# Performance work log

Hardware: AMD Instinct MI355X
Metric: run time of the kernel (lower is better)

Reference implementation:

```python
import jax, jax.numpy as jnp
import numpy as np

N_NODES = 50000
N_EDGES = 800000
IN_CH = 128
HID = 256
OUT_CH = 10
N_GRAPHS = 64


def setup_inputs() -> dict:
    key = jax.random.key(0)
    ks = jax.random.split(key, 16)
    s = 0.02
    inp = {
        "x": jax.random.normal(ks[0], (N_NODES, IN_CH), dtype=jnp.float32),
        "edge_index": jax.random.randint(ks[1], (2, N_EDGES), 0, N_NODES, dtype=jnp.int64),
        "batch": jnp.sort(jax.random.randint(ks[2], (N_NODES,), 0, N_GRAPHS, dtype=jnp.int64)),
        # SAGEConv params: out = lin_l(mean_agg) + lin_r(x_root); lin_l has bias, lin_r does not (PyG default)
        "W1l": jax.random.normal(ks[3], (HID, IN_CH), dtype=jnp.float32) * s,
        "b1": jnp.zeros((HID,), jnp.float32),
        "W1r": jax.random.normal(ks[4], (HID, IN_CH), dtype=jnp.float32) * s,
        "W2l": jax.random.normal(ks[5], (HID, HID), dtype=jnp.float32) * s,
        "b2": jnp.zeros((HID,), jnp.float32),
        "W2r": jax.random.normal(ks[6], (HID, HID), dtype=jnp.float32) * s,
        "W3l": jax.random.normal(ks[7], (HID, HID), dtype=jnp.float32) * s,
        "b3": jnp.zeros((HID,), jnp.float32),
        "W3r": jax.random.normal(ks[8], (HID, HID), dtype=jnp.float32) * s,
        "lin1_W": jax.random.normal(ks[9], (HID // 2, HID), dtype=jnp.float32) * s,
        "lin1_b": jnp.zeros((HID // 2,), jnp.float32),
        "lin2_W": jax.random.normal(ks[10], (OUT_CH, HID // 2), dtype=jnp.float32) * s,
        "lin2_b": jnp.zeros((OUT_CH,), jnp.float32),
    }
    return inp


def _sage_conv(x, src, dst, Wl, bl, Wr):
    # mean-aggregate neighbor features at destination nodes
    msg_sum = jax.ops.segment_sum(x[src], dst, num_segments=N_NODES)  # [N, d]
    deg = jax.ops.segment_sum(jnp.ones((src.shape[0],), x.dtype), dst, num_segments=N_NODES)
    agg = msg_sum / jnp.maximum(deg, 1.0)[:, None]
    return agg @ Wl.T + bl + x @ Wr.T


def reference(x, edge_index, batch, W1l, b1, W1r, W2l, b2, W2r, W3l, b3, W3r,
              lin1_W, lin1_b, lin2_W, lin2_b):
    src, dst = edge_index[0], edge_index[1]
    h = jax.nn.relu(_sage_conv(x, src, dst, W1l, b1, W1r))
    h = jax.nn.relu(_sage_conv(h, src, dst, W2l, b2, W2r))
    h = jax.nn.relu(_sage_conv(h, src, dst, W3l, b3, W3r))
    # global_mean_pool over batch vector
    pooled_sum = jax.ops.segment_sum(h, batch, num_segments=N_GRAPHS)  # [G, HID]
    counts = jax.ops.segment_sum(jnp.ones((h.shape[0],), h.dtype), batch, num_segments=N_GRAPHS)
    g = pooled_sum / jnp.maximum(counts, 1.0)[:, None]
    g = jax.nn.relu(g @ lin1_W.T + lin1_b)
    # dropout is identity in eval mode
    return g @ lin2_W.T + lin2_b
```

## Files before the change

kernel.cpp:

```cpp
#include <hip/hip_runtime.h>
#include <hip/hip_bf16.h>


#define HID 256
typedef unsigned short ushort_t;
typedef __bf16 bf16x8 __attribute__((ext_vector_type(8)));
typedef float  f32x4  __attribute__((ext_vector_type(4)));
typedef float  f32x2  __attribute__((ext_vector_type(2)));

__device__ __forceinline__ unsigned short f2bf(float f) {
    unsigned int u = __float_as_uint(f);
    unsigned int r = (u + 0x7fffu + ((u >> 16) & 1u)) >> 16;
    return (unsigned short)r;
}
__device__ __forceinline__ float bflo(unsigned int u) { return __uint_as_float(u << 16); }
__device__ __forceinline__ float bfhi(unsigned int u) { return __uint_as_float(u & 0xffff0000u); }
__device__ __forceinline__ unsigned int packbf(float a, float b) {
    return (unsigned int)f2bf(a) | ((unsigned int)f2bf(b) << 16);
}
__device__ __forceinline__ void gld16(const void* g, void* l) {
    __builtin_amdgcn_global_load_lds(
        (const __attribute__((address_space(1))) unsigned int*)g,
        (__attribute__((address_space(3))) unsigned int*)l, 16, 0, 0);
}
__device__ __forceinline__ void fma8(float* a, float w, const uint4 v) {
    a[0] = fmaf(w, bflo(v.x), a[0]); a[1] = fmaf(w, bfhi(v.x), a[1]);
    a[2] = fmaf(w, bflo(v.y), a[2]); a[3] = fmaf(w, bfhi(v.y), a[3]);
    a[4] = fmaf(w, bflo(v.z), a[4]); a[5] = fmaf(w, bfhi(v.z), a[5]);
    a[6] = fmaf(w, bflo(v.w), a[6]); a[7] = fmaf(w, bfhi(v.w), a[7]);
}
__device__ __forceinline__ void fma8_f8(float* a, float w, const uint2 v) {
    const f32x2 c01 = __builtin_amdgcn_cvt_pk_f32_fp8(v.x, false);
    const f32x2 c23 = __builtin_amdgcn_cvt_pk_f32_fp8(v.x, true);
    const f32x2 c45 = __builtin_amdgcn_cvt_pk_f32_fp8(v.y, false);
    const f32x2 c67 = __builtin_amdgcn_cvt_pk_f32_fp8(v.y, true);
    a[0] = fmaf(w, c01.x, a[0]); a[1] = fmaf(w, c01.y, a[1]);
    a[2] = fmaf(w, c23.x, a[2]); a[3] = fmaf(w, c23.y, a[3]);
    a[4] = fmaf(w, c45.x, a[4]); a[5] = fmaf(w, c45.y, a[5]);
    a[6] = fmaf(w, c67.x, a[6]); a[7] = fmaf(w, c67.y, a[7]);
}
__device__ __forceinline__ int4 load4idx(const int* __restrict__ csr, int pbase, int e1m1) {
    int4 r;
    r.x = csr[min(pbase + 0, e1m1)];
    r.y = csr[min(pbase + 1, e1m1)];
    r.z = csr[min(pbase + 2, e1m1)];
    r.w = csr[min(pbase + 3, e1m1)];
    return r;
}

#define NBUCK 256
#define NPB_BUCK 196
#define BCAP 4096

__global__ __launch_bounds__(256)
void cvt_kernel(const float* __restrict__ x, ushort_t* __restrict__ xb,
                unsigned char* __restrict__ x8, int nx4,
                const float* __restrict__ W1l, const float* __restrict__ W1r,
                const float* __restrict__ W2l, const float* __restrict__ W2r,
                const float* __restrict__ W3l, const float* __restrict__ W3r,
                ushort_t* __restrict__ wdst, int s1, int s2,
                int* __restrict__ bcursor, float* __restrict__ pooled) {
    const int t = blockIdx.x * 256 + threadIdx.x;
    if (t < NBUCK) bcursor[t] = 0;
    if (t < 64 * 256 / 4) *(float4*)(pooled + t * 4) = make_float4(0.f, 0.f, 0.f, 0.f);
    if (t < nx4) {
        const int i = t * 4;
        const float4 v = *(const float4*)(x + i);
        *(uint2*)(xb + i) = make_uint2(packbf(v.x, v.y), packbf(v.z, v.w));
        int p = __builtin_amdgcn_cvt_pk_fp8_f32(v.x, v.y, 0, false);
        p = __builtin_amdgcn_cvt_pk_fp8_f32(v.z, v.w, p, true);
        *(unsigned int*)(x8 + i) = (unsigned int)p;
        return;
    }
    int off = t - nx4;
    const int total = 2 * s1 + 4 * s2;
    if (off >= total) return;
    const int i = off;
    const float* src;
    if (off < s1) src = W1l;
    else if ((off -= s1) < s1) src = W1r;
    else if ((off -= s1) < s2) src = W2l;
    else if ((off -= s2) < s2) src = W2r;
    else if ((off -= s2) < s2) src = W3l;
    else { off -= s2; src = W3r; }
    wdst[i] = f2bf(src[off]);
}

__global__ __launch_bounds__(256)
void binA_kernel(const int* __restrict__ src, const int* __restrict__ dst,
                 int* __restrict__ bcursor, unsigned int* __restrict__ staging, int E) {
    __shared__ int hist[NBUCK];
    __shared__ int wbase[NBUCK];
    const int tid = threadIdx.x;
    hist[tid] = 0;
    __syncthreads();
    const int i0 = blockIdx.x * 2048;
    int d8[8], s8[8], b8[8];
    #pragma unroll
    for (int j = 0; j < 8; ++j) {
        const int i = i0 + j * 256 + tid;
        if (i < E) {
            d8[j] = dst[i];
            s8[j] = src[i];
            b8[j] = d8[j] / NPB_BUCK;
            atomicAdd(&hist[b8[j]], 1);
        } else b8[j] = -1;
    }
    __syncthreads();
    {
        const int b = tid;
        const int cnt = hist[b];
        int wb = 0;
        if (cnt > 0) wb = atomicAdd(&bcursor[b], cnt);
        wbase[b] = b * BCAP + wb;
        hist[b] = 0;
    }
    __syncthreads();
    #pragma unroll
    for (int j = 0; j < 8; ++j) {
        if (b8[j] >= 0) {
            const int pos = wbase[b8[j]] + atomicAdd(&hist[b8[j]], 1);
            if (pos < (b8[j] + 1) * BCAP)
                staging[pos] = ((unsigned int)(d8[j] - b8[j] * NPB_BUCK) << 16) | (unsigned int)s8[j];
        }
    }
}

__global__ __launch_bounds__(256)
void binB_kernel(const unsigned int* __restrict__ staging, const int* __restrict__ bcursor,
                 int* __restrict__ csr, int* __restrict__ offsets, int nn, int E) {
    __shared__ unsigned int sedge[BCAP];
    __shared__ int cnt[NBUCK];
    __shared__ int bsum[4];
    __shared__ int wt[4];
    const int b = blockIdx.x, tid = threadIdx.x;
    const int lane = tid & 63, wid = tid >> 6;

    int part = (tid < b) ? bcursor[tid] : 0;
    #pragma unroll
    for (int d = 1; d < 64; d <<= 1) part += __shfl_xor(part, d, 64);
    if (lane == 0) bsum[wid] = part;
    const int mycnt = min(bcursor[b], BCAP);
    __syncthreads();
    const int base = bsum[0] + bsum[1] + bsum[2] + bsum[3];

    for (int i = tid; i < mycnt; i += 256) sedge[i] = staging[b * BCAP + i];
    cnt[tid] = 0;
    __syncthreads();
    for (int i = tid; i < mycnt; i += 256) atomicAdd(&cnt[sedge[i] >> 16], 1);
    __syncthreads();

    const int v = cnt[tid];
    int incl = v;
    #pragma unroll
    for (int d = 1; d < 64; d <<= 1) {
        int t = __shfl_up(incl, d, 64);
        if (lane >= d) incl += t;
    }
    if (lane == 63) wt[wid] = incl;
    __syncthreads();
    int wb = 0;
    #pragma unroll
    for (int w = 0; w < 4; ++w) { int t = wt[w]; if (w < wid) wb += t; }
    const int excl = wb + incl - v;

    const int node = b * NPB_BUCK + tid;
    if (tid < NPB_BUCK && node < nn) offsets[node] = base + excl;
    if (b == NBUCK - 1 && tid == 0) offsets[nn] = E;
    __syncthreads();
    cnt[tid] = excl;
    __syncthreads();

    for (int i = tid; i < mycnt; i += 256) {
        const unsigned int e = sedge[i];
        const int p = atomicAdd(&cnt[e >> 16], 1);
        csr[base + p] = (int)(e & 0xFFFFu);
    }
}

template <int C>
__global__ __launch_bounds__(256)
void agg8_kernel(const unsigned char* __restrict__ h8, const int* __restrict__ offsets,
                 const int* __restrict__ csr, ushort_t* __restrict__ out, int nn) {
    constexpr int CL = C / 8;
    constexpr int EW = 64 / CL;
    constexpr int RPE = 4 * EW;
    const int node = (blockIdx.x * 256 + threadIdx.x) >> 6;
    if (node >= nn) return;
    const int lane = threadIdx.x & 63;
    const int cl = lane & (CL - 1);
    const int eo = lane / CL;
    const int e0 = offsets[node], e1 = offsets[node + 1];
    const int deg = e1 - e0;
    const int rounds = (deg + RPE - 1) / RPE;
    const int e1m1 = max(e1 - 1, 0);
    float a[8] = {0.f, 0.f, 0.f, 0.f, 0.f, 0.f, 0.f, 0.f};
    int pb = e0 + eo * 4;
    if (rounds > 0) {
        int4 idx = load4idx(csr, pb, e1m1);
        for (int r2 = 0; r2 < rounds; ++r2) {
            const int4 cur = idx;
            const int pcur = pb;
            pb += RPE;
            if (r2 + 1 < rounds) idx = load4idx(csr, pb, e1m1);
            const uint2 v0 = *(const uint2*)(h8 + (size_t)cur.x * C + cl * 8);
            const uint2 v1 = *(const uint2*)(h8 + (size_t)cur.y * C + cl * 8);
            const uint2 v2 = *(const uint2*)(h8 + (size_t)cur.z * C + cl * 8);
            const uint2 v3 = *(const uint2*)(h8 + (size_t)cur.w * C + cl * 8);
            fma8_f8(a, (pcur + 0 < e1) ? 1.f : 0.f, v0);
            fma8_f8(a, (pcur + 1 < e1) ? 1.f : 0.f, v1);
            fma8_f8(a, (pcur + 2 < e1) ? 1.f : 0.f, v2);
            fma8_f8(a, (pcur + 3 < e1) ? 1.f : 0.f, v3);
        }
    }
    #pragma unroll
    for (int d = CL; d < 64; d <<= 1)
        #pragma unroll
        for (int r = 0; r < 8; ++r) a[r] += __shfl_xor(a[r], d, 64);
    if (eo == 0) {
        const float inv = 1.0f / fmaxf((float)deg, 1.0f);
        uint4 o;
        o.x = packbf(a[0] * inv, a[1] * inv);
        o.y = packbf(a[2] * inv, a[3] * inv);
        o.z = packbf(a[4] * inv, a[5] * inv);
        o.w = packbf(a[6] * inv, a[7] * inv);
        *(uint4*)(out + (size_t)node * C + cl * 8) = o;
    }
}

template <int K, bool W8>
__global__ __launch_bounds__(256, 2)
void gemm2_mfma(const ushort_t* __restrict__ A1, const ushort_t* __restrict__ A2,
                const ushort_t* __restrict__ W1, const ushort_t* __restrict__ W2,
                const float* __restrict__ bias, ushort_t* __restrict__ Cout,
                unsigned char* __restrict__ H8, int M) {
    __shared__ ushort_t As[2 * 128 * 64];
    __shared__ ushort_t Bs[2 * 128 * 64];
    const int tid = threadIdx.x;
    const int row0 = blockIdx.x * 128, col0 = blockIdx.y * 128;
    const int wave = tid >> 6, lane = tid & 63;
    const int wm = (wave & 1) * 64, wn = (wave >> 1) * 64;
    const int l15 = lane & 15, quad = lane >> 4;
    constexpr int NCH = K / 128;

    f32x4 acc[4][4] = {};

    #pragma unroll
    for (int phase = 0; phase < 2; ++phase) {
        const ushort_t* __restrict__ A = phase ? A2 : A1;
        const ushort_t* __restrict__ W = phase ? W2 : W1;
        for (int kc = 0; kc < NCH; ++kc) {
            const int kt = kc * 128;
            __syncthreads();
            #pragma unroll
            for (int p = 0; p < 8; ++p) {
                const int slot = p * 256 + tid;
                const int g = slot >> 10;
                const int r = (slot >> 3) & 127;
                const int c = slot & 7;
                const int cg = c ^ (r & 7);
                int ar = row0 + r; if (ar >= M) ar = M - 1;
                gld16(A + (size_t)ar * K + kt + g * 64 + cg * 8, &As[slot * 8]);
            }
            #pragma unroll
            for (int p = 0; p < 8; ++p) {
                const int slot = p * 256 + tid;
                const int g = slot >> 10;
                const int r = (slot >> 3) & 127;
                const int c = slot & 7;
                const int cg = c ^ (r & 7);
                gld16(W + (size_t)(col0 + r) * K + kt + g * 64 + cg * 8, &Bs[slot * 8]);
            }
            __syncthreads();
            #pragma unroll
            for (int g = 0; g < 2; ++g) {
                #pragma unroll
                for (int ks = 0; ks < 2; ++ks) {
                    const int kq = ks * 4 + quad;
                    bf16x8 af[4], bfv[4];
                    #pragma unroll
                    for (int i = 0; i < 4; ++i) {
                        const int r = wm + i * 16 + l15;
                        const int cl = kq ^ (r & 7);
                        af[i] = *(const bf16x8*)&As[g * 8192 + r * 64 + cl * 8];
                    }
                    #pragma unroll
                    for (int j = 0; j < 4; ++j) {
                        const int r = wn + j * 16 + l15;
                        const int cl = kq ^ (r & 7);
                        bfv[j] = *(const bf16x8*)&Bs[g * 8192 + r * 64 + cl * 8];
                    }
                    #pragma unroll
                    for (int i = 0; i < 4; ++i)
                        #pragma unroll
                        for (int j = 0; j < 4; ++j)
                            acc[i][j] = __builtin_amdgcn_mfma_f32_16x16x32_bf16(
                                af[i], bfv[j], acc[i][j], 0, 0, 0);
                }
            }
        }
    }

    #pragma unroll
    for (int i = 0; i < 4; ++i) {
        const int mbase = row0 + wm + i * 16 + quad * 4;
        #pragma unroll
        for (int j = 0; j < 4; ++j) {
            const int n = col0 + wn + j * 16 + l15;
            const float b = bias[n];
            #pragma unroll
            for (int reg = 0; reg < 4; ++reg) {
                const int mr = mbase + reg;
                const float v = fmaxf(acc[i][j][reg] + b, 0.f);
                const float vp = __shfl_xor(v, 1, 64);
                if (!(l15 & 1) && mr < M)
                    *(unsigned int*)(Cout + (size_t)mr * 256 + n) = packbf(v, vp);
                if (W8) {
                    const int p2 = __builtin_amdgcn_cvt_pk_fp8_f32(v, vp, 0, false);
                    const int q2 = __shfl_xor(p2, 2, 64);
                    if ((l15 & 3) == 0 && mr < M)
                        *(unsigned int*)(H8 + (size_t)mr * 256 + n) =
                            ((unsigned int)p2 & 0xFFFFu) | ((unsigned int)q2 << 16);
                }
            }
        }
    }
}

__global__ __launch_bounds__(256)
void pool_partial_kernel(const ushort_t* __restrict__ h, const int* __restrict__ batch,
                         float* __restrict__ pooled, int nn) {
    const int n0 = blockIdx.x * 64;
    if (n0 >= nn) return;
    const int n1 = min(n0 + 64, nn);
    const int tid = threadIdx.x;
    const int cl = tid & 31, rg = tid >> 5;
    const int g0 = batch[n0];
    const int g1 = batch[n1 - 1];
    float a0[8] = {0.f, 0.f, 0.f, 0.f, 0.f, 0.f, 0.f, 0.f};
    float a1[8] = {0.f, 0.f, 0.f, 0.f, 0.f, 0.f, 0.f, 0.f};
    for (int n = n0 + rg; n < n1; n += 8) {
        const uint4 v = *(const uint4*)(h + (size_t)n * 256 + cl * 8);
        const float w1 = (batch[n] != g0) ? 1.f : 0.f;
        fma8(a0, 1.f - w1, v);
        fma8(a1, w1, v);
    }
    __shared__ float red[8][512];
    #pragma unroll
    for (int r = 0; r < 8; ++r) {
        red[rg][cl * 8 + r] = a0[r];
        red[rg][256 + cl * 8 + r] = a1[r];
    }
    __syncthreads();
    float s0 = 0.f, s1 = 0.f;
    #pragma unroll
    for (int r = 0; r < 8; ++r) { s0 += red[r][tid]; s1 += red[r][256 + tid]; }
    atomicAdd(&pooled[g0 * 256 + tid], s0);
    if (g1 != g0) atomicAdd(&pooled[g1 * 256 + tid], s1);
}

__global__ __launch_bounds__(256)
void mlp_kernel(const float* __restrict__ pooled, const int* __restrict__ batch, int nn,
                const float* __restrict__ lin1W, const float* __restrict__ lin1b,
                const float* __restrict__ lin2W, const float* __restrict__ lin2b,
                float* __restrict__ out) {
    const int g = blockIdx.x;
    const int tid = threadIdx.x;
    int lo = 0, hi = nn;
    while (lo < hi) { int mid = (lo + hi) >> 1; if (batch[mid] < g) lo = mid + 1; else hi = mid; }
    const int s = lo;
    hi = nn;
    while (lo < hi) { int mid = (lo + hi) >> 1; if (batch[mid] < g + 1) lo = mid + 1; else hi = mid; }
    const int e = lo;
    __shared__ float meanv[256];
    __shared__ float g1v[128];
    meanv[tid] = pooled[g * 256 + tid] / fmaxf((float)(e - s), 1.0f);
    __syncthreads();
    if (tid < 128) {
        float acc = lin1b[tid];
        #pragma unroll 4
        for (int k = 0; k < 256; k += 4) {
            const float4 w = *(const float4*)(lin1W + tid * 256 + k);
            acc += meanv[k] * w.x + meanv[k + 1] * w.y + meanv[k + 2] * w.z + meanv[k + 3] * w.w;
        }
        g1v[tid] = fmaxf(acc, 0.f);
    }
    __syncthreads();
    if (tid < 10) {
        float o = lin2b[tid];
        #pragma unroll 4
        for (int k = 0; k < 128; k += 4) {
            const float4 w = *(const float4*)(lin2W + tid * 128 + k);
            o += g1v[k] * w.x + g1v[k + 1] * w.y + g1v[k + 2] * w.z + g1v[k + 3] * w.w;
        }
        out[g * 10 + tid] = o;
    }
}

extern "C" void kernel_launch(void* const* d_in, const int* in_sizes, int n_in,
                              void* d_out, int out_size, void* d_ws, size_t ws_size,
                              hipStream_t stream) {
    const float* x     = (const float*)d_in[0];
    const int*   eidx  = (const int*)d_in[1];
    const int*   batch = (const int*)d_in[2];
    const float* W1l = (const float*)d_in[3];
    const float* b1  = (const float*)d_in[4];
    const float* W1r = (const float*)d_in[5];
    const float* W2l = (const float*)d_in[6];
    const float* b2  = (const float*)d_in[7];
    const float* W2r = (const float*)d_in[8];
    const float* W3l = (const float*)d_in[9];
    const float* b3  = (const float*)d_in[10];
    const float* W3r = (const float*)d_in[11];
    const float* lin1W = (const float*)d_in[12];
    const float* lin1b = (const float*)d_in[13];
    const float* lin2W = (const float*)d_in[14];
    const float* lin2b = (const float*)d_in[15];
    float* out = (float*)d_out;

    const int E  = in_sizes[1] / 2;
    const int NN = in_sizes[2];
    const int IN = 128;
    const int* src = eidx;
    const int* dst = eidx + E;

    char* ws = (char*)d_ws;
    size_t off = 0;
    auto alloc = [&](size_t bytes) { void* p = ws + off; off += (bytes + 255) / 256 * 256; return p; };
    ushort_t* xb  = (ushort_t*)alloc((size_t)NN * IN * 2);
    unsigned char* x8 = (unsigned char*)alloc((size_t)NN * IN);
    ushort_t* agg = (ushort_t*)alloc((size_t)NN * HID * 2);
    ushort_t* hA  = (ushort_t*)alloc((size_t)NN * HID * 2);
    ushort_t* hB  = (ushort_t*)alloc((size_t)NN * HID * 2);
    unsigned char* h8 = (unsigned char*)alloc((size_t)NN * HID);
    const int s1 = HID * IN, s2 = HID * HID;
    ushort_t* wb  = (ushort_t*)alloc((size_t)(2 * s1 + 4 * s2) * 2);
    int* offsets   = (int*)alloc((size_t)(NN + 1) * 4);
    int* csr       = (int*)alloc((size_t)E * 4);
    unsigned int* staging = (unsigned int*)alloc((size_t)NBUCK * BCAP * 4);
    int* bcursor   = (int*)alloc(NBUCK * 4);
    float* pooled  = (float*)alloc(64 * 256 * 4);
    (void)ws_size; (void)n_in; (void)out_size;

    const ushort_t* W1lb = wb;
    const ushort_t* W1rb = wb + s1;
    const ushort_t* W2lb = wb + 2 * s1;
    const ushort_t* W2rb = wb + 2 * s1 + s2;
    const ushort_t* W3lb = wb + 2 * s1 + 2 * s2;
    const ushort_t* W3rb = wb + 2 * s1 + 3 * s2;

    const int TB = 256;
    const int mgrid = (NN + 127) / 128;

    const int nx4 = NN * IN / 4;
    const int wtotal = 2 * s1 + 4 * s2;
    cvt_kernel<<<(nx4 + wtotal + TB - 1) / TB, TB, 0, stream>>>(
        x, xb, x8, nx4, W1l, W1r, W2l, W2r, W3l, W3r, wb, s1, s2, bcursor, pooled);

    binA_kernel<<<(E + 2047) / 2048, TB, 0, stream>>>(src, dst, bcursor, staging, E);
    binB_kernel<<<NBUCK, TB, 0, stream>>>(staging, bcursor, csr, offsets, NN, E);

    agg8_kernel<128><<<(NN + 3) / 4, TB, 0, stream>>>(x8, offsets, csr, agg, NN);
    gemm2_mfma<128, true><<<dim3(mgrid, 2), TB, 0, stream>>>(agg, xb, W1lb, W1rb, b1, hA, h8, NN);
    agg8_kernel<256><<<(NN + 3) / 4, TB, 0, stream>>>(h8, offsets, csr, agg, NN);
    gemm2_mfma<256, true><<<dim3(mgrid, 2), TB, 0, stream>>>(agg, hA, W2lb, W2rb, b2, hB, h8, NN);
    agg8_kernel<256><<<(NN + 3) / 4, TB, 0, stream>>>(h8, offsets, csr, agg, NN);
    gemm2_mfma<256, false><<<dim3(mgrid, 2), TB, 0, stream>>>(agg, hB, W3lb, W3rb, b3, hA, nullptr, NN);

    pool_partial_kernel<<<(NN + 63) / 64, TB, 0, stream>>>(hA, batch, pooled, NN);
    mlp_kernel<<<64, TB, 0, stream>>>(pooled, batch, NN, lin1W, lin1b, lin2W, lin2b, out);
}
```

Before: 324.8 us.

## Store all activations and aggregates in fp8, decode to bf16 inside GEMM

Switches every intermediate tensor (aggregates, root features, layer outputs) from bf16 to fp8 storage. The GEMM now loads fp8 A tiles into a smaller LDS buffer and decodes them to bf16 before the MFMA, which cuts A-operand traffic and LDS use and allows raising occupancy to 3 blocks per CU. This drops the dual bf16/fp8 writes in the epilogue and the bf16 copy of x. It adds decode ALU work in the inner loop and lowers precision of the root-path and final activations, which risks accuracy.

```diff
diff --git a/kernel.cpp b/kernel.cpp
--- a/kernel.cpp
+++ b/kernel.cpp
@@ -22,12 +22,6 @@
     __builtin_amdgcn_global_load_lds(
         (const __attribute__((address_space(1))) unsigned int*)g,
         (__attribute__((address_space(3))) unsigned int*)l, 16, 0, 0);
-}
-__device__ __forceinline__ void fma8(float* a, float w, const uint4 v) {
-    a[0] = fmaf(w, bflo(v.x), a[0]); a[1] = fmaf(w, bfhi(v.x), a[1]);
-    a[2] = fmaf(w, bflo(v.y), a[2]); a[3] = fmaf(w, bfhi(v.y), a[3]);
-    a[4] = fmaf(w, bflo(v.z), a[4]); a[5] = fmaf(w, bfhi(v.z), a[5]);
-    a[6] = fmaf(w, bflo(v.w), a[6]); a[7] = fmaf(w, bfhi(v.w), a[7]);
 }
 __device__ __forceinline__ void fma8_f8(float* a, float w, const uint2 v) {
     const f32x2 c01 = __builtin_amdgcn_cvt_pk_f32_fp8(v.x, false);
@@ -39,6 +33,18 @@
     a[4] = fmaf(w, c45.x, a[4]); a[5] = fmaf(w, c45.y, a[5]);
     a[6] = fmaf(w, c67.x, a[6]); a[7] = fmaf(w, c67.y, a[7]);
 }
+__device__ __forceinline__ bf16x8 dec8(const uint2 v) {
+    const f32x2 c01 = __builtin_amdgcn_cvt_pk_f32_fp8(v.x, false);
+    const f32x2 c23 = __builtin_amdgcn_cvt_pk_f32_fp8(v.x, true);
+    const f32x2 c45 = __builtin_amdgcn_cvt_pk_f32_fp8(v.y, false);
+    const f32x2 c67 = __builtin_amdgcn_cvt_pk_f32_fp8(v.y, true);
+    uint4 u;
+    u.x = packbf(c01.x, c01.y);
+    u.y = packbf(c23.x, c23.y);
+    u.z = packbf(c45.x, c45.y);
+    u.w = packbf(c67.x, c67.y);
+    return *(bf16x8*)&u;
+}
 __device__ __forceinline__ int4 load4idx(const int* __restrict__ csr, int pbase, int e1m1) {
     int4 r;
     r.x = csr[min(pbase + 0, e1m1)];
@@ -53,8 +59,7 @@
 #define BCAP 4096
 
 __global__ __launch_bounds__(256)
-void cvt_kernel(const float* __restrict__ x, ushort_t* __restrict__ xb,
-                unsigned char* __restrict__ x8, int nx4,
+void cvt_kernel(const float* __restrict__ x, unsigned char* __restrict__ x8, int nx4,
                 const float* __restrict__ W1l, const float* __restrict__ W1r,
                 const float* __restrict__ W2l, const float* __restrict__ W2r,
                 const float* __restrict__ W3l, const float* __restrict__ W3r,
@@ -66,7 +71,6 @@
     if (t < nx4) {
         const int i = t * 4;
         const float4 v = *(const float4*)(x + i);
-        *(uint2*)(xb + i) = make_uint2(packbf(v.x, v.y), packbf(v.z, v.w));
         int p = __builtin_amdgcn_cvt_pk_fp8_f32(v.x, v.y, 0, false);
         p = __builtin_amdgcn_cvt_pk_fp8_f32(v.z, v.w, p, true);
         *(unsigned int*)(x8 + i) = (unsigned int)p;
@@ -181,7 +185,7 @@
 template <int C>
 __global__ __launch_bounds__(256)
 void agg8_kernel(const unsigned char* __restrict__ h8, const int* __restrict__ offsets,
-                 const int* __restrict__ csr, ushort_t* __restrict__ out, int nn) {
+                 const int* __restrict__ csr, unsigned char* __restrict__ out, int nn) {
     constexpr int CL = C / 8;
     constexpr int EW = 64 / CL;
     constexpr int RPE = 4 * EW;
@@ -219,22 +223,20 @@
         for (int r = 0; r < 8; ++r) a[r] += __shfl_xor(a[r], d, 64);
     if (eo == 0) {
         const float inv = 1.0f / fmaxf((float)deg, 1.0f);
-        uint4 o;
-        o.x = packbf(a[0] * inv, a[1] * inv);
-        o.y = packbf(a[2] * inv, a[3] * inv);
-        o.z = packbf(a[4] * inv, a[5] * inv);
-        o.w = packbf(a[6] * inv, a[7] * inv);
-        *(uint4*)(out + (size_t)node * C + cl * 8) = o;
-    }
-}
-
-template <int K, bool W8>
-__global__ __launch_bounds__(256, 2)
-void gemm2_mfma(const ushort_t* __restrict__ A1, const ushort_t* __restrict__ A2,
+        int p = __builtin_amdgcn_cvt_pk_fp8_f32(a[0] * inv, a[1] * inv, 0, false);
+        p = __builtin_amdgcn_cvt_pk_fp8_f32(a[2] * inv, a[3] * inv, p, true);
+        int q = __builtin_amdgcn_cvt_pk_fp8_f32(a[4] * inv, a[5] * inv, 0, false);
+        q = __builtin_amdgcn_cvt_pk_fp8_f32(a[6] * inv, a[7] * inv, q, true);
+        *(uint2*)(out + (size_t)node * C + cl * 8) = make_uint2((unsigned int)p, (unsigned int)q);
+    }
+}
+
+template <int K>
+__global__ __launch_bounds__(256, 3)
+void gemm2_mfma(const unsigned char* __restrict__ A1, const unsigned char* __restrict__ A2,
                 const ushort_t* __restrict__ W1, const ushort_t* __restrict__ W2,
-                const float* __restrict__ bias, ushort_t* __restrict__ Cout,
-                unsigned char* __restrict__ H8, int M) {
-    __shared__ ushort_t As[2 * 128 * 64];
+                const float* __restrict__ bias, unsigned char* __restrict__ H8, int M) {
+    __shared__ unsigned char As8[128 * 128];
     __shared__ ushort_t Bs[2 * 128 * 64];
     const int tid = threadIdx.x;
     const int row0 = blockIdx.x * 128, col0 = blockIdx.y * 128;
@@ -247,20 +249,18 @@
 
     #pragma unroll
     for (int phase = 0; phase < 2; ++phase) {
-        const ushort_t* __restrict__ A = phase ? A2 : A1;
+        const unsigned char* __restrict__ A = phase ? A2 : A1;
         const ushort_t* __restrict__ W = phase ? W2 : W1;
         for (int kc = 0; kc < NCH; ++kc) {
             const int kt = kc * 128;
             __syncthreads();
             #pragma unroll
-            for (int p = 0; p < 8; ++p) {
+            for (int p = 0; p < 4; ++p) {
                 const int slot = p * 256 + tid;
-                const int g = slot >> 10;
-                const int r = (slot >> 3) & 127;
-                const int c = slot & 7;
+                const int r = slot >> 3, c = slot & 7;
                 const int cg = c ^ (r & 7);
                 int ar = row0 + r; if (ar >= M) ar = M - 1;
-                gld16(A + (size_t)ar * K + kt + g * 64 + cg * 8, &As[slot * 8]);
+                gld16(A + (size_t)ar * K + kt + cg * 16, &As8[slot * 16]);
             }
             #pragma unroll
             for (int p = 0; p < 8; ++p) {
@@ -277,12 +277,14 @@
                 #pragma unroll
                 for (int ks = 0; ks < 2; ++ks) {
                     const int kq = ks * 4 + quad;
+                    const int idx = g * 8 + kq;
+                    const int ci = idx >> 1, half = idx & 1;
                     bf16x8 af[4], bfv[4];
                     #pragma unroll
                     for (int i = 0; i < 4; ++i) {
                         const int r = wm + i * 16 + l15;
-                        const int cl = kq ^ (r & 7);
-                        af[i] = *(const bf16x8*)&As[g * 8192 + r * 64 + cl * 8];
+                        const uint2 va = *(const uint2*)&As8[r * 128 + (ci ^ (r & 7)) * 16 + half * 8];
+                        af[i] = dec8(va);
                     }
                     #pragma unroll
                     for (int j = 0; j < 4; ++j) {
@@ -313,22 +315,18 @@
                 const int mr = mbase + reg;
                 const float v = fmaxf(acc[i][j][reg] + b, 0.f);
                 const float vp = __shfl_xor(v, 1, 64);
-                if (!(l15 & 1) && mr < M)
-                    *(unsigned int*)(Cout + (size_t)mr * 256 + n) = packbf(v, vp);
-                if (W8) {
-                    const int p2 = __builtin_amdgcn_cvt_pk_fp8_f32(v, vp, 0, false);
-                    const int q2 = __shfl_xor(p2, 2, 64);
-                    if ((l15 & 3) == 0 && mr < M)
-                        *(unsigned int*)(H8 + (size_t)mr * 256 + n) =
-                            ((unsigned int)p2 & 0xFFFFu) | ((unsigned int)q2 << 16);
-                }
+                const int p2 = __builtin_amdgcn_cvt_pk_fp8_f32(v, vp, 0, false);
+                const int q2 = __shfl_xor(p2, 2, 64);
+                if ((l15 & 3) == 0 && mr < M)
+                    *(unsigned int*)(H8 + (size_t)mr * 256 + n) =
+                        ((unsigned int)p2 & 0xFFFFu) | ((unsigned int)q2 << 16);
             }
         }
     }
 }
 
 __global__ __launch_bounds__(256)
-void pool_partial_kernel(const ushort_t* __restrict__ h, const int* __restrict__ batch,
+void pool_partial_kernel(const unsigned char* __restrict__ h8, const int* __restrict__ batch,
                          float* __restrict__ pooled, int nn) {
     const int n0 = blockIdx.x * 64;
     if (n0 >= nn) return;
@@ -340,10 +338,10 @@
     float a0[8] = {0.f, 0.f, 0.f, 0.f, 0.f, 0.f, 0.f, 0.f};
     float a1[8] = {0.f, 0.f, 0.f, 0.f, 0.f, 0.f, 0.f, 0.f};
     for (int n = n0 + rg; n < n1; n += 8) {
-        const uint4 v = *(const uint4*)(h + (size_t)n * 256 + cl * 8);
+        const uint2 v = *(const uint2*)(h8 + (size_t)n * 256 + cl * 8);
         const float w1 = (batch[n] != g0) ? 1.f : 0.f;
-        fma8(a0, 1.f - w1, v);
-        fma8(a1, w1, v);
+        fma8_f8(a0, 1.f - w1, v);
+        fma8_f8(a1, w1, v);
     }
     __shared__ float red[8][512];
     #pragma unroll
@@ -427,12 +425,11 @@
     char* ws = (char*)d_ws;
     size_t off = 0;
     auto alloc = [&](size_t bytes) { void* p = ws + off; off += (bytes + 255) / 256 * 256; return p; };
-    ushort_t* xb  = (ushort_t*)alloc((size_t)NN * IN * 2);
-    unsigned char* x8 = (unsigned char*)alloc((size_t)NN * IN);
-    ushort_t* agg = (ushort_t*)alloc((size_t)NN * HID * 2);
-    ushort_t* hA  = (ushort_t*)alloc((size_t)NN * HID * 2);
-    ushort_t* hB  = (ushort_t*)alloc((size_t)NN * HID * 2);
-    unsigned char* h8 = (unsigned char*)alloc((size_t)NN * HID);
+    unsigned char* x8   = (unsigned char*)alloc((size_t)NN * IN);
+    unsigned char* agg8 = (unsigned char*)alloc((size_t)NN * HID);
+    unsigned char* h8a  = (unsigned char*)alloc((size_t)NN * HID);
+    unsigned char* h8b  = (unsigned char*)alloc((size_t)NN * HID);
+    unsigned char* h8c  = (unsigned char*)alloc((size_t)NN * HID);
     const int s1 = HID * IN, s2 = HID * HID;
     ushort_t* wb  = (ushort_t*)alloc((size_t)(2 * s1 + 4 * s2) * 2);
     int* offsets   = (int*)alloc((size_t)(NN + 1) * 4);
@@ -455,18 +452,18 @@
     const int nx4 = NN * IN / 4;
     const int wtotal = 2 * s1 + 4 * s2;
     cvt_kernel<<<(nx4 + wtotal + TB - 1) / TB, TB, 0, stream>>>(
-        x, xb, x8, nx4, W1l, W1r, W2l, W2r, W3l, W3r, wb, s1, s2, bcursor, pooled);
+        x, x8, nx4, W1l, W1r, W2l, W2r, W3l, W3r, wb, s1, s2, bcursor, pooled);
 
     binA_kernel<<<(E + 2047) / 2048, TB, 0, stream>>>(src, dst, bcursor, staging, E);
     binB_kernel<<<NBUCK, TB, 0, stream>>>(staging, bcursor, csr, offsets, NN, E);
 
-    agg8_kernel<128><<<(NN + 3) / 4, TB, 0, stream>>>(x8, offsets, csr, agg, NN);
-    gemm2_mfma<128, true><<<dim3(mgrid, 2), TB, 0, stream>>>(agg, xb, W1lb, W1rb, b1, hA, h8, NN);
-    agg8_kernel<256><<<(NN + 3) / 4, TB, 0, stream>>>(h8, offsets, csr, agg, NN);
-    gemm2_mfma<256, true><<<dim3(mgrid, 2), TB, 0, stream>>>(agg, hA, W2lb, W2rb, b2, hB, h8, NN);
-    agg8_kernel<256><<<(NN + 3) / 4, TB, 0, stream>>>(h8, offsets, csr, agg, NN);
-    gemm2_mfma<256, false><<<dim3(mgrid, 2), TB, 0, stream>>>(agg, hB, W3lb, W3rb, b3, hA, nullptr, NN);
-
-    pool_partial_kernel<<<(NN + 63) / 64, TB, 0, stream>>>(hA, batch, pooled, NN);
+    agg8_kernel<128><<<(NN + 3) / 4, TB, 0, stream>>>(x8, offsets, csr, agg8, NN);
+    gemm2_mfma<128><<<dim3(mgrid, 2), TB, 0, stream>>>(agg8, x8, W1lb, W1rb, b1, h8a, NN);
+    agg8_kernel<256><<<(NN + 3) / 4, TB, 0, stream>>>(h8a, offsets, csr, agg8, NN);
+    gemm2_mfma<256><<<dim3(mgrid, 2), TB, 0, stream>>>(agg8, h8a, W2lb, W2rb, b2, h8b, NN);
+    agg8_kernel<256><<<(NN + 3) / 4, TB, 0, stream>>>(h8b, offsets, csr, agg8, NN);
+    gemm2_mfma<256><<<dim3(mgrid, 2), TB, 0, stream>>>(agg8, h8b, W3lb, W3rb, b3, h8c, NN);
+
+    pool_partial_kernel<<<(NN + 63) / 64, TB, 0, stream>>>(h8c, batch, pooled, NN);
     mlp_kernel<<<64, TB, 0, stream>>>(pooled, batch, NN, lin1W, lin1b, lin2W, lin2b, out);
 }
```

Result: slower. 331.9 us (+2.2%).
